# Kernel optimization log

Measured on AMD Instinct MI355X. Metric: run time of the kernel, lower is better.

## Reference

```python
import jax, jax.numpy as jnp
import numpy as np

NUM_SEGMENTS = 8192  # number of graphs/segments (B); batch ids are in [0, B)
N = 8388608          # total nodes


def setup_inputs() -> dict:
    key = jax.random.key(0)
    k1, k2 = jax.random.split(key)
    x = jax.random.normal(k1, (N,), dtype=jnp.float32)
    batch = jnp.sort(jax.random.randint(k2, (N,), 0, NUM_SEGMENTS))
    return {"x": x, "batch": batch}


def _sparsemax(x, batch):
    n = x.shape[0]
    # per-segment max subtraction (shift invariance / numerical stability)
    seg_max = jax.ops.segment_max(x, batch, num_segments=NUM_SEGMENTS)
    xs = x - seg_max[batch]

    # segmented descending sort: primary key = batch, secondary = -x
    order = jnp.lexsort((-xs, batch))
    sx = xs[order]          # sorted values, segment-contiguous, descending within segment
    sb = batch[order]       # == sorted batch ids

    # segment sizes and start offsets
    num_nodes = jax.ops.segment_sum(jnp.ones_like(batch), batch, num_segments=NUM_SEGMENTS)
    cum = jnp.concatenate([jnp.zeros((1,), num_nodes.dtype), jnp.cumsum(num_nodes)[:-1]])

    # within-segment 1-based rank (rhos) and within-segment cumsum
    start = cum[sb]
    rhos = (jnp.arange(n) - start + 1).astype(x.dtype)
    c = jnp.cumsum(sx)
    base = jnp.where(start > 0, c[jnp.maximum(start - 1, 0)], jnp.zeros((), x.dtype))
    seg_cumsum = c - base

    # sparsemax support: rho * z_sorted > cumsum - 1
    support = rhos * sx > seg_cumsum - 1.0
    supp_size = jax.ops.segment_sum(support.astype(num_nodes.dtype), sb, num_segments=NUM_SEGMENTS)

    # threshold tau per segment: (cumsum at support boundary - 1) / support_size
    idx = jnp.clip(cum + supp_size - 1, 0, n - 1)
    tau = (seg_cumsum[idx] - 1.0) / jnp.maximum(supp_size, 1).astype(x.dtype)

    return jnp.maximum(xs - tau[batch], 0.0)


def reference(x, batch):
    return _sparsemax(x, batch)
```

## Files before the change

### kernel.cpp

```cpp
#include <hip/hip_runtime.h>


#define NSEG   8192
#define NTOT   8388608
#define L1N    524288
#define L2N    32768
#define L3N    2048
#define PADV   (-3.0e38f)
#define WREG   1216
#define FBB    256

__device__ __forceinline__ int esw(const int e) {
    return (e & ~15) | ((e + (e >> 4)) & 15);
}

__device__ __forceinline__ void cs(float& a, float& b, const bool up) {
    const float lo = fminf(a, b), hi = fmaxf(a, b);
    a = up ? hi : lo;
    b = up ? lo : hi;
}

__device__ __forceinline__ void sort4(float r[4], const int gib) {
    cs(r[0], r[1], true);  cs(r[2], r[3], false);
    const bool u4 = ((gib & 4) == 0);
    cs(r[0], r[2], u4); cs(r[1], r[3], u4);
    cs(r[0], r[1], u4); cs(r[2], r[3], u4);
}

template<int K>
__device__ __forceinline__ void bmerge4(float r[4], const int gib) {
    const bool up = ((gib & K) == 0);
    #pragma unroll
    for (int j = K >> 1; j >= 4; j >>= 1) {
        const bool tkm = (up == ((gib & j) == 0));
        const int tm = j >> 2;
        #pragma unroll
        for (int m = 0; m < 4; ++m) {
            const float p = __shfl_xor(r[m], tm, 64);
            r[m] = tkm ? fmaxf(r[m], p) : fminf(r[m], p);
        }
    }
    #pragma unroll
    for (int j = 2; j >= 1; j >>= 1)
        #pragma unroll
        for (int m = 0; m < 4; ++m)
            if ((m & j) == 0) cs(r[m], r[m | j], up);
}

template<int K, int J>
__device__ __forceinline__ void cepm(float r[16]) {
    #pragma unroll
    for (int m = 0; m < 16; ++m)
        if ((m & J) == 0) { const bool up = ((m & K) == 0); cs(r[m], r[m | J], up); }
}
template<int J>
__device__ __forceinline__ void cep(float r[16], const bool up) {
    #pragma unroll
    for (int m = 0; m < 16; ++m)
        if ((m & J) == 0) cs(r[m], r[m | J], up);
}
template<int KD>
__device__ __forceinline__ void kphase16(float r[16], const int l) {
    const bool up = ((l & (KD >> 4)) == 0);
    #pragma unroll
    for (int tm = KD >> 5; tm >= 1; tm >>= 1) {
        const bool tkm = (up == ((l & tm) == 0));
        #pragma unroll
        for (int m = 0; m < 16; ++m) {
            const float p = __shfl_xor(r[m], tm, 64);
            r[m] = tkm ? fmaxf(r[m], p) : fminf(r[m], p);
        }
    }
    cep<8>(r, up); cep<4>(r, up); cep<2>(r, up); cep<1>(r, up);
}
__device__ __forceinline__ void wsort1024(float r[16], const int l) {
    cepm<2, 1>(r);
    cepm<4, 2>(r); cepm<4, 1>(r);
    cepm<8, 4>(r); cepm<8, 2>(r); cepm<8, 1>(r);
    kphase16<16>(r, l);  kphase16<32>(r, l);  kphase16<64>(r, l);
    kphase16<128>(r, l); kphase16<256>(r, l); kphase16<512>(r, l);
    kphase16<1024>(r, l);
}

__global__ __launch_bounds__(256) void k1_bounds(
    const int* __restrict__ batch, int* __restrict__ starts, const int n)
{
    const int i = blockIdx.x * blockDim.x + threadIdx.x;
    if (i >= n) return;
    const int bi = batch[i];
    int bp = __shfl_up(bi, 1, 64);
    if (((threadIdx.x & 63) == 0) && i > 0) bp = batch[i - 1];
    if (i == 0) { for (int b = 0; b <= bi; ++b) starts[b] = 0; }
    else {
        for (int b = bp + 1; b <= bi; ++b) starts[b] = i;
    }
    if (i == n - 1) { for (int b = bi + 1; b <= NSEG; ++b) starts[b] = n; }
}

__global__ __launch_bounds__(256) void k2w(
    const float* __restrict__ x, const int* __restrict__ starts,
    float* __restrict__ mx_out, float* __restrict__ S, float* __restrict__ L1)
{
    __shared__ __align__(16) float Wall[4 * WREG];
    const int tid  = threadIdx.x;
    const int lane = tid & 63;
    const int wid  = tid >> 6;
    float* W = Wall + wid * WREG;

    const int b = blockIdx.x * 4 + wid;
    const int s = starts[b], e = starts[b + 1];
    const int n = e - s;
    if (n <= 0) { if (lane == 0) mx_out[b] = 0.0f; return; }

    const bool med = (n > 1024);
    const int  nb  = n - 1024;

    float r[16], rb[4];
    #pragma unroll
    for (int m = 0; m < 16; ++m) { const int i = 16 * lane + m; r[m] = (i < n) ? x[s + i] : PADV; }
    if (med) {
        #pragma unroll
        for (int m = 0; m < 4; ++m) { const int i = 1024 + 4 * lane + m; rb[m] = (i < n) ? x[s + i] : PADV; }
    }

    float mx = r[0];
    #pragma unroll
    for (int m = 1; m < 16; ++m) mx = fmaxf(mx, r[m]);
    if (med) {
        #pragma unroll
        for (int m = 0; m < 4; ++m) mx = fmaxf(mx, rb[m]);
    }
    #pragma unroll
    for (int o = 32; o; o >>= 1) mx = fmaxf(mx, __shfl_xor(mx, o, 64));
    if (lane == 0) mx_out[b] = mx;

    #pragma unroll
    for (int m = 0; m < 16; ++m) r[m] = r[m] - mx;
    if (med) {
        #pragma unroll
        for (int m = 0; m < 4; ++m) rb[m] = rb[m] - mx;
    }

    wsort1024(r, lane);

    if (med) {
        const int gib = 4 * lane;
        sort4(rb, gib);
        bmerge4<8>(rb, gib);   bmerge4<16>(rb, gib);  bmerge4<32>(rb, gib);
        bmerge4<64>(rb, gib);  bmerge4<128>(rb, gib); bmerge4<256>(rb, gib);

        float tu[16];
        #pragma unroll
        for (int m = 0; m < 16; ++m) {
            const int k  = ((63 - lane) << 4) + (15 - m);
            const int sk = (k >> 2) & 63;
            const float pv = __shfl(rb[(15 - m) & 3], sk, 64);
            const float hi = fmaxf(r[m], pv);
            const float lo = fminf(r[m], pv);
            const bool act = (lane >= 48);
            tu[m] = act ? lo : PADV;
            r[m]  = act ? hi : r[m];
        }
        kphase16<1024>(r, lane);
        #pragma unroll
        for (int tm = 8; tm >= 1; tm >>= 1) {
            #pragma unroll
            for (int m = 0; m < 16; ++m) {
                const float p = __shfl_xor(tu[m], tm, 64);
                const bool tkm = ((lane & tm) == 0);
                tu[m] = tkm ? fmaxf(tu[m], p) : fminf(tu[m], p);
            }
        }
        cep<8>(tu, true); cep<4>(tu, true); cep<2>(tu, true); cep<1>(tu, true);

        #pragma unroll
        for (int m = 0; m < 16; ++m) W[esw(16 * lane + m)] = r[m];
        if (lane >= 48) {
            const int t0 = (lane - 48) << 4;
            #pragma unroll
            for (int m = 0; m < 16; ++m) {
                const int t = t0 + m;
                if (t < nb && t < 192) W[esw(1024 + t)] = tu[m];
            }
        }
    } else {
        #pragma unroll
        for (int m = 0; m < 16; ++m) W[esw(16 * lane + m)] = r[m];
    }

    for (int i = lane; i < n; i += 64) S[s + i] = W[esw(i)];

    const int q0 = (s + 15) >> 4, q1 = e >> 4;
    for (int rr = lane; rr < q1 - q0; rr += 64) {
        const int lb = ((q0 + rr) << 4) - s;
        float v[16];
        #pragma unroll
        for (int ii = 0; ii < 16; ++ii) v[ii] = W[esw(lb + ii)];
        float a = 0.0f;
        #pragma unroll
        for (int ii = 0; ii < 16; ++ii) a = a + v[ii];
        L1[q0 + rr] = a;
    }
}

__global__ __launch_bounds__(256) void kM1(
    const float* __restrict__ S, const int* __restrict__ starts,
    float* __restrict__ L1, float* __restrict__ L2, float* __restrict__ L3)
{
    __shared__ float l2s[256];
    __shared__ int sbr[2];
    const int k = blockIdx.x, tid = threadIdx.x;

    if (tid < 2) {
        const int target = 65536 * (k + tid);
        int lo = 0, hi = NSEG;
        while (lo < hi) { const int mid = (lo + hi) >> 1; if (starts[mid] < target) lo = mid + 1; else hi = mid; }
        sbr[tid] = lo;
    }
    __syncthreads();
    for (int b = sbr[0] + tid; b < sbr[1]; b += 256) {
        const int s = starts[b];
        if (s & 15) {
            const int q = s >> 4;
            const float* p = S + ((size_t)q << 4);
            float a = 0.0f;
            #pragma unroll
            for (int i = 0; i < 16; ++i) a = a + p[i];
            L1[q] = a;
        }
    }
    __syncthreads();

    const int q2 = (k << 8) + tid;
    {
        const float* p = L1 + ((size_t)q2 << 4);
        float a = 0.0f;
        #pragma unroll
        for (int i = 0; i < 16; ++i) a = a + p[i];
        L2[q2] = a;
        l2s[tid] = a;
    }
    __syncthreads();
    if (tid < 16) {
        float a = 0.0f;
        #pragma unroll
        for (int i = 0; i < 16; ++i) a = a + l2s[(tid << 4) + i];
        L3[(k << 4) + tid] = a;
    }
}

__global__ __launch_bounds__(256) void kB(const float* __restrict__ L1,
                                          const float* __restrict__ L2,
                                          const float* __restrict__ L3g,
                                          float* __restrict__ C1)
{
    __shared__ float l3[L3N], c3[L3N], l4[128], c4[128], l5[8], c5[8], c2s[256];
    const int k = blockIdx.x, tid = threadIdx.x;

    for (int q = tid; q < L3N; q += 256) l3[q] = L3g[q];
    __syncthreads();
    if (tid < 128) {
        float a = 0.0f;
        for (int i = 0; i < 16; ++i) a = a + l3[tid * 16 + i];
        l4[tid] = a;
    }
    __syncthreads();
    if (tid < 8) {
        float a = 0.0f;
        for (int i = 0; i < 16; ++i) a = a + l4[tid * 16 + i];
        l5[tid] = a;
    }
    __syncthreads();
    if (tid == 0) {
        float a = 0.0f;
        for (int i = 0; i < 8; ++i) { a = a + l5[i]; c5[i] = a; }
    }
    __syncthreads();
    if (tid < 8) {
        const float pre = tid ? c5[tid - 1] : 0.0f;
        float a = 0.0f;
        for (int i = 0; i < 16; ++i) { a = a + l4[tid * 16 + i]; c4[tid * 16 + i] = tid ? (a + pre) : a; }
    }
    __syncthreads();
    if (tid < 128) {
        const float pre = tid ? c4[tid - 1] : 0.0f;
        float a = 0.0f;
        for (int i = 0; i < 16; ++i) { a = a + l3[tid * 16 + i]; c3[tid * 16 + i] = tid ? (a + pre) : a; }
    }
    __syncthreads();
    if (tid < 16) {
        const int q2r = (k << 4) + tid;
        const float pre = q2r ? c3[q2r - 1] : 0.0f;
        const float* p = L2 + ((size_t)q2r << 4);
        float a = 0.0f;
        #pragma unroll
        for (int i = 0; i < 16; ++i) { a = a + p[i]; c2s[(tid << 4) + i] = q2r ? (a + pre) : a; }
    }
    __syncthreads();
    {
        const int p1 = (k << 8) + 1 + tid;
        if (p1 < L2N) {
            const float pre = c2s[tid];
            const float* pL = L1 + ((size_t)p1 << 4);
            float a = 0.0f;
            #pragma unroll
            for (int i = 0; i < 16; ++i) { a = a + pL[i]; C1[((size_t)p1 << 4) + i] = a + pre; }
        }
        if (k == 0 && tid == 0) {
            float a = 0.0f;
            #pragma unroll
            for (int i = 0; i < 16; ++i) { a = a + L1[i]; C1[i] = a; }
        }
    }
}

__device__ __forceinline__ float c_row(const int j, const float* __restrict__ S,
                                       const float* __restrict__ C1)
{
    const int q = j >> 4;
    const float* p = S + ((size_t)q << 4);
    float a = 0.0f;
    for (int i = 0; i <= (j & 15); ++i) a = a + p[i];
    return q ? (a + C1[q - 1]) : a;
}

__global__ __launch_bounds__(64) void kCF(
    const float* __restrict__ x, const float* __restrict__ S, const float* __restrict__ C1,
    const int* __restrict__ starts, const int* __restrict__ batch,
    const float* __restrict__ mx, float* __restrict__ out)
{
    const int b = blockIdx.x, lane = threadIdx.x;
    const int s = starts[b], e = starts[b + 1];
    const int n = e - s;
    if (n <= 0) return;

    float base = 0.0f;
    if (lane == 0 && s > 0) base = c_row(s - 1, S, C1);
    base = __shfl(base, 0, 64);

    const int q0 = s >> 4;
    const int nrows = ((e - 1) >> 4) - q0 + 1;
    const int R = (nrows < 32) ? nrows : 32;

    int cnt = 0;
    for (int rr = lane; rr < R; rr += 64) {
        const int q = q0 + rr;
        const float pre = q ? C1[q - 1] : 0.0f;
        float vals[16];
        const float4* p4 = (const float4*)(S + ((size_t)q << 4));
        #pragma unroll
        for (int v = 0; v < 4; ++v) {
            const float4 f = p4[v];
            vals[4 * v + 0] = f.x; vals[4 * v + 1] = f.y;
            vals[4 * v + 2] = f.z; vals[4 * v + 3] = f.w;
        }
        float a = 0.0f;
        #pragma unroll
        for (int i = 0; i < 16; ++i) {
            a = a + vals[i];
            const int j = (q << 4) + i;
            if (j >= s && j < e) {
                const float cj  = q ? (a + pre) : a;
                const float seg = (cj - base) - 1.0f;
                const float lhs = (float)(j - s + 1) * vals[i];
                if (lhs > seg) cnt++;
            }
        }
    }
    #pragma unroll
    for (int o = 32; o; o >>= 1) cnt += __shfl_xor(cnt, o, 64);
    const int supp = cnt;

    float t = 0.0f;
    if (lane == 0) {
        if (supp > 0) {
            const int idx = s + supp - 1;
            const float ci = c_row(idx, S, C1);
            t = ((ci - base) - 1.0f) / (float)supp;
        } else {
            const int g  = batch[s - 1];
            const int sg = starts[g];
            const float bg = (sg > 0) ? c_row(sg - 1, S, C1) : 0.0f;
            t = (base - bg) - 1.0f;
        }
    }
    t = __shfl(t, 0, 64);
    const float tb = t;
    const float mxb = mx[b];
    for (int i = s + lane; i < e; i += 64) {
        float v = x[i] - mxb;
        v = v - tb;
        out[i] = v > 0.0f ? v : 0.0f;
    }
}

__global__ void k_base(const float* __restrict__ S, const float* __restrict__ C1,
                       const int* __restrict__ starts,
                       float* __restrict__ baseA, float* __restrict__ rowP)
{
    const int b = blockIdx.x * blockDim.x + threadIdx.x;
    if (b >= NSEG) return;
    const int s = starts[b];
    float P = 0.0f, base = 0.0f;
    if (s > 0) {
        const int j = s - 1;
        const int q = j >> 4;
        const float* p = S + ((size_t)q << 4);
        float a = 0.0f;
        for (int i = 0; i <= (j & 15); ++i) a = a + p[i];
        if (s & 15) P = a;
        base = q ? (a + C1[q - 1]) : a;
    }
    baseA[b] = base;
    rowP[b] = P;
}

__global__ __launch_bounds__(128) void kC(
    const float* __restrict__ x, const float* __restrict__ S, const float* __restrict__ C1,
    const int* __restrict__ starts, const int* __restrict__ batch,
    const float* __restrict__ mx, const float* __restrict__ baseA,
    const float* __restrict__ rowP, float* __restrict__ out)
{
    __shared__ float stau[1];
    __shared__ int   scnt[2];

    const int b = blockIdx.x, tid = threadIdx.x;
    const int s = starts[b], e = starts[b + 1];
    const int n = e - s;
    if (n <= 0) return;

    const float base = baseA[b];
    const int q0 = s >> 4;
    const int nrows = ((e - 1) >> 4) - q0 + 1;
    const int R = (nrows < 32) ? nrows : 32;

    int cnt = 0;
    for (int rr = tid; rr < R; rr += 128) {
        const int q = q0 + rr;
        const float pre = q ? C1[q - 1] : 0.0f;
        float vals[16];
        const float4* p4 = (const float4*)(S + ((size_t)q << 4));
        #pragma unroll
        for (int v = 0; v < 4; ++v) {
            const float4 f = p4[v];
            vals[4 * v + 0] = f.x; vals[4 * v + 1] = f.y;
            vals[4 * v + 2] = f.z; vals[4 * v + 3] = f.w;
        }
        float a = (rr == 0) ? rowP[b] : 0.0f;
        const int i0 = (rr == 0) ? (s & 15) : 0;
        #pragma unroll
        for (int i = 0; i < 16; ++i) {
            if (i >= i0) {
                a = a + vals[i];
                const int j = (q << 4) + i;
                if (j < e) {
                    const float cj  = q ? (a + pre) : a;
                    const float seg = (cj - base) - 1.0f;
                    const float lhs = (float)(j - s + 1) * vals[i];
                    if (lhs > seg) cnt++;
                }
            }
        }
    }
    #pragma unroll
    for (int o = 32; o; o >>= 1) cnt += __shfl_xor(cnt, o, 64);
    if ((tid & 63) == 0) scnt[tid >> 6] = cnt;
    __syncthreads();
    const int supp = scnt[0] + scnt[1];

    if (tid == 0) {
        float t;
        if (supp > 0) {
            const int idx = s + supp - 1;
            const int qi = idx >> 4;
            const float* p = S + ((size_t)qi << 4);
            float a = (qi == q0) ? rowP[b] : 0.0f;
            const int i0 = (qi == q0) ? (s & 15) : 0;
            for (int i = i0; i <= (idx & 15); ++i) a = a + p[i];
            const float ci = qi ? (a + C1[qi - 1]) : a;
            t = ((ci - base) - 1.0f) / (float)supp;
        } else {
            int idx = s - 1; if (idx < 0) idx = 0;
            const int g = batch[idx];
            t = (base - baseA[g]) - 1.0f;
        }
        stau[0] = t;
    }
    __syncthreads();
    const float tb = stau[0];
    const float mxb = mx[b];
    for (int i = s + tid; i < e; i += 128) {
        float v = x[i] - mxb;
        v = v - tb;
        out[i] = v > 0.0f ? v : 0.0f;
    }
}

__global__ void fb_sparsemax(const float* x, const int* batch, float* out, int n_total)
{
    __shared__ float sred[FBB];
    __shared__ int   sredi[FBB];
    __shared__ int   sb2[2];
    const int tid = threadIdx.x;
    const int b = blockIdx.x;
    if (tid == 0) {
        int lo = 0, hi = n_total;
        while (lo < hi) { int mid = (lo + hi) >> 1; if (batch[mid] < b) lo = mid + 1; else hi = mid; }
        sb2[0] = lo; hi = n_total;
        while (lo < hi) { int mid = (lo + hi) >> 1; if (batch[mid] < b + 1) lo = mid + 1; else hi = mid; }
        sb2[1] = lo;
    }
    __syncthreads();
    const int s = sb2[0], e = sb2[1], n = e - s;
    if (n <= 0) return;
    float mx = -3.0e38f;
    for (int i = s + tid; i < e; i += FBB) { float v = x[i]; if (v > mx) mx = v; }
    sred[tid] = mx; __syncthreads();
    for (int o = FBB / 2; o > 0; o >>= 1) { if (tid < o && sred[tid + o] > sred[tid]) sred[tid] = sred[tid + o]; __syncthreads(); }
    mx = sred[0]; __syncthreads();
    float tau = -1.0f; int prev = -1;
    for (int it = 0; it < 64; ++it) {
        float sum = 0.0f; int cnt = 0;
        for (int i = s + tid; i < e; i += FBB) { float v = x[i] - mx; if (v > tau) { sum += v; cnt++; } }
        sred[tid] = sum; sredi[tid] = cnt; __syncthreads();
        for (int o = FBB / 2; o > 0; o >>= 1) { if (tid < o) { sred[tid] += sred[tid + o]; sredi[tid] += sredi[tid + o]; } __syncthreads(); }
        sum = sred[0]; cnt = sredi[0]; __syncthreads();
        if (cnt == prev || cnt == 0) break;
        tau = (sum - 1.0f) / (float)cnt; prev = cnt; __syncthreads();
    }
    for (int i = s + tid; i < e; i += FBB) { float v = x[i] - mx - tau; out[i] = v > 0.0f ? v : 0.0f; }
}
__global__ void fb_sentinel(float* out) { if (threadIdx.x == 0 && blockIdx.x == 0) out[0] = 20000.0f; }

extern "C" void kernel_launch(void* const* d_in, const int* in_sizes, int n_in,
                              void* d_out, int out_size, void* d_ws, size_t ws_size,
                              hipStream_t stream) {
    const float* x     = (const float*)d_in[0];
    const int*   batch = (const int*)d_in[1];
    float*       out   = (float*)d_out;
    float*       wsf   = (float*)d_ws;
    const int n = in_sizes[0];

    const size_t base_f  = (size_t)8448 + 8192 + L1N + L2N + L3N + L1N;
    const size_t small_f = base_f + 8192 + 8192;
    const size_t big_f   = small_f + (size_t)NTOT;
    if (n != NTOT || ws_size < small_f * sizeof(float)) {
        fb_sparsemax<<<NSEG, FBB, 0, stream>>>(x, batch, out, n);
        fb_sentinel<<<1, 64, 0, stream>>>(out);
        return;
    }
    int*   starts = (int*)wsf;
    float* mx     = wsf + 8448;
    float* L1 = mx + 8192;
    float* L2 = L1 + L1N;
    float* L3 = L2 + L2N;
    float* C1 = L3 + L3N;
    float* baseA = C1 + L1N;
    float* rowP  = baseA + 8192;

    const bool big = (ws_size >= big_f * sizeof(float));
    float* S = big ? (rowP + 8192) : out;

    k1_bounds<<<(n + 255) / 256, 256, 0, stream>>>(batch, starts, n);
    k2w<<<NSEG / 4, 256, 0, stream>>>(x, starts, mx, S, L1);
    kM1<<<128, 256, 0, stream>>>(S, starts, L1, L2, L3);
    kB<<<128, 256, 0, stream>>>(L1, L2, L3, C1);
    if (big) {
        kCF<<<NSEG, 64, 0, stream>>>(x, S, C1, starts, batch, mx, out);
    } else {
        k_base<<<NSEG / 256, 256, 0, stream>>>(S, C1, starts, baseA, rowP);
        kC<<<NSEG, 128, 0, stream>>>(x, S, C1, starts, batch, mx, baseA, rowP, out);
    }
}
```

Measured before the change: 207.0 us.

## Vectorize boundary scan, coalesce segment loads, pack four segments per block

The boundary kernel now has each thread read four batch ids with an int4 load and write the segment starts for all four, so it launches a quarter of the threads. In k2w the per-segment loads change from a per-lane contiguous stride to a lane-interleaved stride so wave accesses coalesce. kCF packs four wave-segments into each 256-thread block instead of one segment per 64-thread block. Changing the element-to-register mapping in k2w may not match the bitonic sort's layout assumptions, and the k1 change assumes n is divisible by four.

```diff
diff --git a/kernel.cpp b/kernel.cpp
--- a/kernel.cpp
+++ b/kernel.cpp
@@ -85,16 +85,18 @@
 __global__ __launch_bounds__(256) void k1_bounds(
     const int* __restrict__ batch, int* __restrict__ starts, const int n)
 {
-    const int i = blockIdx.x * blockDim.x + threadIdx.x;
-    if (i >= n) return;
-    const int bi = batch[i];
-    int bp = __shfl_up(bi, 1, 64);
-    if (((threadIdx.x & 63) == 0) && i > 0) bp = batch[i - 1];
-    if (i == 0) { for (int b = 0; b <= bi; ++b) starts[b] = 0; }
-    else {
-        for (int b = bp + 1; b <= bi; ++b) starts[b] = i;
-    }
-    if (i == n - 1) { for (int b = bi + 1; b <= NSEG; ++b) starts[b] = n; }
+    const int t = blockIdx.x * blockDim.x + threadIdx.x;
+    const int i0 = t << 2;
+    if (i0 >= n) return;
+    const int4 b4 = ((const int4*)batch)[t];
+    int bp = __shfl_up(b4.w, 1, 64);
+    if (((threadIdx.x & 63) == 0) && i0 > 0) bp = batch[i0 - 1];
+    if (i0 == 0) { for (int b = 0; b <= b4.x; ++b) starts[b] = 0; }
+    else { for (int b = bp + 1; b <= b4.x; ++b) starts[b] = i0; }
+    for (int b = b4.x + 1; b <= b4.y; ++b) starts[b] = i0 + 1;
+    for (int b = b4.y + 1; b <= b4.z; ++b) starts[b] = i0 + 2;
+    for (int b = b4.z + 1; b <= b4.w; ++b) starts[b] = i0 + 3;
+    if (i0 + 4 == n) { for (int b = b4.w + 1; b <= NSEG; ++b) starts[b] = n; }
 }
 
 __global__ __launch_bounds__(256) void k2w(
@@ -117,10 +119,10 @@
 
     float r[16], rb[4];
     #pragma unroll
-    for (int m = 0; m < 16; ++m) { const int i = 16 * lane + m; r[m] = (i < n) ? x[s + i] : PADV; }
+    for (int m = 0; m < 16; ++m) { const int i = (m << 6) + lane; r[m] = (i < n) ? x[s + i] : PADV; }
     if (med) {
         #pragma unroll
-        for (int m = 0; m < 4; ++m) { const int i = 1024 + 4 * lane + m; rb[m] = (i < n) ? x[s + i] : PADV; }
+        for (int m = 0; m < 4; ++m) { const int i = 1024 + (m << 6) + lane; rb[m] = (i < n) ? x[s + i] : PADV; }
     }
 
     float mx = r[0];
@@ -324,12 +326,13 @@
     return q ? (a + C1[q - 1]) : a;
 }
 
-__global__ __launch_bounds__(64) void kCF(
+__global__ __launch_bounds__(256) void kCF(
     const float* __restrict__ x, const float* __restrict__ S, const float* __restrict__ C1,
     const int* __restrict__ starts, const int* __restrict__ batch,
     const float* __restrict__ mx, float* __restrict__ out)
 {
-    const int b = blockIdx.x, lane = threadIdx.x;
+    const int lane = threadIdx.x & 63;
+    const int b = blockIdx.x * 4 + (threadIdx.x >> 6);
     const int s = starts[b], e = starts[b + 1];
     const int n = e - s;
     if (n <= 0) return;
@@ -561,12 +564,12 @@
     const bool big = (ws_size >= big_f * sizeof(float));
     float* S = big ? (rowP + 8192) : out;
 
-    k1_bounds<<<(n + 255) / 256, 256, 0, stream>>>(batch, starts, n);
+    k1_bounds<<<(n / 4 + 255) / 256, 256, 0, stream>>>(batch, starts, n);
     k2w<<<NSEG / 4, 256, 0, stream>>>(x, starts, mx, S, L1);
     kM1<<<128, 256, 0, stream>>>(S, starts, L1, L2, L3);
     kB<<<128, 256, 0, stream>>>(L1, L2, L3, C1);
     if (big) {
-        kCF<<<NSEG, 64, 0, stream>>>(x, S, C1, starts, batch, mx, out);
+        kCF<<<NSEG / 4, 256, 0, stream>>>(x, S, C1, starts, batch, mx, out);
     } else {
         k_base<<<NSEG / 256, 256, 0, stream>>>(S, C1, starts, baseA, rowP);
         kC<<<NSEG, 128, 0, stream>>>(x, S, C1, starts, batch, mx, baseA, rowP, out);
```

Measured after the change: 196.0 us. 5.3% less time.
